# Optimization experiments

Measured on AMD Instinct MI355X. Metric: run time of the kernel, lower is better.

The kernel has to match this reference:

```python
import jax, jax.numpy as jnp
import numpy as np

N = 512          # pedestrians in scene
T = 12           # decode steps
OBS = 8
FEAT = 2
LAT = 32
COND = 64
LSTM_IN = 128
HID = 64         # lstm_hidden_size == context_state_size
CTX = 64
EMB = 32         # Pooling_net spatial embedding dim
MLP_IN = EMB + 2 * CTX   # 160
MLP_MID = 64
BOT = CTX        # bottleneck_dim = h_dim
IN_DEC = COND + LAT + CTX + FEAT  # 162


def setup_inputs() -> dict:
    key = jax.random.key(0)
    ks = jax.random.split(key, 24)
    s = 0.1
    return {
        "last_position": jax.random.normal(ks[0], (N, FEAT), jnp.float32),
        "c": jax.random.normal(ks[1], (N, COND), jnp.float32),
        "z": jax.random.normal(ks[2], (N, LAT), jnp.float32),
        "obs_traj_pos": jax.random.normal(ks[3], (OBS, N, FEAT), jnp.float32),
        "nei_index": jax.random.randint(ks[4], (T, N, N), 0, 2, jnp.int32),
        "nei_num_index": jax.random.randint(ks[5], (N,), 0, N, jnp.int32),
        "h0": jax.random.normal(ks[6], (N, HID), jnp.float32),
        "c0": jax.random.normal(ks[7], (N, HID), jnp.float32),
        "eps": jax.random.normal(ks[8], (T, N, FEAT), jnp.float32),
        "W_in": jax.random.normal(ks[9], (IN_DEC, LSTM_IN), jnp.float32) * s,
        "b_in": jnp.zeros((LSTM_IN,), jnp.float32),
        "W_ih": jax.random.normal(ks[10], (4 * HID, LSTM_IN), jnp.float32) * s,
        "W_hh": jax.random.normal(ks[11], (4 * HID, HID), jnp.float32) * s,
        "b_ih": jnp.zeros((4 * HID,), jnp.float32),
        "b_hh": jnp.zeros((4 * HID,), jnp.float32),
        "W_l2p": jax.random.normal(ks[12], (HID // 2 + CTX, FEAT), jnp.float32) * s,
        "b_l2p": jnp.zeros((FEAT,), jnp.float32),
        "W_sp": jax.random.normal(ks[13], (FEAT, EMB), jnp.float32) * s,
        "b_sp": jnp.zeros((EMB,), jnp.float32),
        "W1": jax.random.normal(ks[14], (MLP_IN, MLP_MID), jnp.float32) * s,
        "b1": jnp.zeros((MLP_MID,), jnp.float32),
        "W2": jax.random.normal(ks[15], (MLP_MID, BOT), jnp.float32) * s,
        "b2": jnp.zeros((BOT,), jnp.float32),
    }


def reference(last_position, c, z, obs_traj_pos, nei_index, nei_num_index,
              h0, c0, eps, W_in, b_in, W_ih, W_hh, b_ih, b_hh,
              W_l2p, b_l2p, W_sp, b_sp, W1, b1, W2, b2):
    sg = jax.lax.stop_gradient
    half = HID // 2
    neg_inf = jnp.float32(-jnp.inf)

    def pooling(mask, lstm_state, pos):
        # mask: [N,N] bool; lstm_state: [N,CTX]; pos: [N,2]
        corr = pos[:, None, :] - pos[None, :, :]           # [N,N,2] pos[i]-pos[j]
        r = corr @ W_sp + b_sp                              # [N,N,EMB]
        hj = jnp.broadcast_to(lstm_state[None, :, :], (N, N, CTX))
        hi = jnp.broadcast_to(lstm_state[:, None, :], (N, N, CTX))
        x = jnp.concatenate([r, hj, hi], axis=-1)           # [N,N,160]
        h1 = jax.nn.relu(x @ W1 + b1)
        h2 = jax.nn.relu(h1 @ W2 + b2)                      # [N,N,BOT]
        Hm = jnp.where(mask[:, :, None], h2, neg_inf)       # scatter of valid rows
        pool = Hm.max(axis=1)                               # max over neighbors j
        return jnp.where(pool == neg_inf, 0.0, pool)

    def lstm_cell(x, h, cs):
        gates = x @ W_ih.T + b_ih + h @ W_hh.T + b_hh
        i, f, g, o = jnp.split(gates, 4, axis=-1)
        c_new = jax.nn.sigmoid(f) * cs + jax.nn.sigmoid(i) * jnp.tanh(g)
        h_new = jax.nn.sigmoid(o) * jnp.tanh(c_new)
        return h_new, c_new

    def step(carry, xs):
        prev_pos, h, cs, ctx, cur_abs = carry
        nei_t, eps_t = xs
        emb = jnp.concatenate([sg(prev_pos), sg(c), sg(z), sg(ctx)], axis=-1)
        x = jax.nn.relu(emb @ W_in + b_in)
        h, cs = lstm_cell(x, h, cs)
        ctx = pooling(nei_t > 0, h, cur_abs)
        mu = jnp.concatenate([h[:, :half], ctx], -1) @ W_l2p + b_l2p
        logvar = jnp.concatenate([h[:, half:], ctx], -1) @ W_l2p + b_l2p
        pos = mu + eps_t * jnp.exp(0.5 * logvar)
        cur_abs = sg(cur_abs + pos)
        return (pos, h, cs, ctx, cur_abs), (pos, mu, logvar)

    ctx0 = jnp.zeros((N, CTX), jnp.float32)
    carry0 = (last_position, h0, c0, ctx0, obs_traj_pos[-1])
    _, (pre_pos, mean, var) = jax.lax.scan(step, carry0, (nei_index, eps))
    return pre_pos, mean, var
```

## Files before the change

kernel.cpp:

```cpp
#include <hip/hip_runtime.h>
#include <math.h>

#define NP 512
#define TT 12

typedef float f32x4 __attribute__((ext_vector_type(4)));
typedef __bf16 bf16x8 __attribute__((ext_vector_type(8)));

#define OFF_CURABS 0
#define OFF_Q      2048
#define OFF_P      67584
#define OFF_WIHT   100352
#define OFF_WHHT   133120
#define OFF_WC     149504
#define OFF_BASE   149632
#define OFF_H      149696
#define OFF_CS     182464

__global__ __launch_bounds__(256) void init_k(
    const float* __restrict__ obs, const float* __restrict__ W_ih,
    const float* __restrict__ W_hh, const float* __restrict__ W_sp,
    const float* __restrict__ b_sp, const float* __restrict__ W1,
    const float* __restrict__ b1, float* __restrict__ ws) {
  int tid = blockIdx.x * 256 + threadIdx.x;
  if (tid < 1024) ws[OFF_CURABS + tid] = obs[7 * 1024 + tid];
  if (tid < 32768) {
    int k = tid >> 8, g = tid & 255;
    ws[OFF_WIHT + tid] = W_ih[g * 128 + k];
  }
  if (tid < 16384) {
    int k = tid >> 8, g = tid & 255;
    ws[OFF_WHHT + tid] = W_hh[g * 64 + k];
  }
  if (tid < 128) {
    int d = tid >> 6, m = tid & 63;
    float s = 0.f;
    for (int e = 0; e < 32; ++e) s = fmaf(W_sp[d * 32 + e], W1[e * 64 + m], s);
    ws[OFF_WC + tid] = s;
  }
  if (tid < 64) {
    float s = b1[tid];
    for (int e = 0; e < 32; ++e) s = fmaf(b_sp[e], W1[e * 64 + tid], s);
    ws[OFF_BASE + tid] = s;
  }
}

__global__ __launch_bounds__(256) void step_k(
    const float* __restrict__ lastpos, const float* __restrict__ cc,
    const float* __restrict__ zz, const int* __restrict__ nei,
    const float* __restrict__ h0, const float* __restrict__ c0,
    const float* __restrict__ obs, const float* __restrict__ epsin,
    const float* __restrict__ W_in, const float* __restrict__ b_in,
    const float* __restrict__ b_ih, const float* __restrict__ b_hh,
    const float* __restrict__ Wl2p, const float* __restrict__ bl2p,
    const float* __restrict__ W1, const float* __restrict__ W2,
    const float* __restrict__ b2,
    float* __restrict__ out, float* __restrict__ ws, int s) {
  __shared__ __align__(16) __bf16 W2T[64 * 72];
  __shared__ int   ml[512];
  __shared__ float wcl[128], basev[64];
  __shared__ float red[4][64];
  __shared__ float hloc[64], csloc[64], ctxloc[64], prevp[2], pxy[2];
  __shared__ float emb[162], xpart[2][128], xvec[128], gl[256];

  int t = threadIdx.x;
  int b = blockIdx.x;
  int lane = t & 63, w = t >> 6;
  int quad = lane >> 4, col = lane & 15;

  if (t < 64) {
    if (s == 0) { hloc[t] = h0[b * 64 + t]; csloc[t] = c0[b * 64 + t]; ctxloc[t] = 0.f; }
    else        { hloc[t] = ws[OFF_H + b * 64 + t]; csloc[t] = ws[OFF_CS + b * 64 + t]; }
    basev[t] = ws[OFF_BASE + t];
  } else if (t < 192) {
    wcl[t - 64] = ws[OFF_WC + (t - 64)];
  }
  if (s == 0 && t < 2) {
    prevp[t] = lastpos[b * 2 + t];
    pxy[t]   = obs[7 * 1024 + b * 2 + t];
  }
  if (s > 0) {
    for (int e = t; e < 4096; e += 256)
      W2T[(e & 63) * 72 + (e >> 6)] = (__bf16)W2[e];
    const int* neirow = nei + ((size_t)(s - 1) * NP + b) * NP;
    for (int j = t; j < 512; j += 256) ml[j] = neirow[j];
  }
  __syncthreads();

  if (s > 0) {
    int st = s - 1;
    const float* Qb = ws + OFF_Q + (st & 1) * 32768;
    bf16x8 bf00 = *(const bf16x8*)&W2T[(0 * 16 + col) * 72 + 0 * 32 + quad * 8];
    bf16x8 bf01 = *(const bf16x8*)&W2T[(0 * 16 + col) * 72 + 1 * 32 + quad * 8];
    bf16x8 bf10 = *(const bf16x8*)&W2T[(1 * 16 + col) * 72 + 0 * 32 + quad * 8];
    bf16x8 bf11 = *(const bf16x8*)&W2T[(1 * 16 + col) * 72 + 1 * 32 + quad * 8];
    bf16x8 bf20 = *(const bf16x8*)&W2T[(2 * 16 + col) * 72 + 0 * 32 + quad * 8];
    bf16x8 bf21 = *(const bf16x8*)&W2T[(2 * 16 + col) * 72 + 1 * 32 + quad * 8];
    bf16x8 bf30 = *(const bf16x8*)&W2T[(3 * 16 + col) * 72 + 0 * 32 + quad * 8];
    bf16x8 bf31 = *(const bf16x8*)&W2T[(3 * 16 + col) * 72 + 1 * 32 + quad * 8];
    float pl0[8], pl1[8];
    #pragma unroll
    for (int e = 0; e < 8; ++e) {
      pl0[e] = ws[OFF_P + b * 64 + quad * 8 + e];
      pl1[e] = ws[OFF_P + b * 64 + 32 + quad * 8 + e];
    }
    float vmax0 = -1e30f, vmax1 = -1e30f, vmax2 = -1e30f, vmax3 = -1e30f;

    for (int c = 0; c < 8; ++c) {
      int j0 = w * 128 + c * 16;
      int jr = (j0 + col) * 64 + quad * 8;
      f32x4 qa = *(const f32x4*)&Qb[jr];
      f32x4 qb = *(const f32x4*)&Qb[jr + 4];
      f32x4 qc = *(const f32x4*)&Qb[jr + 32];
      f32x4 qd = *(const f32x4*)&Qb[jr + 36];
      bf16x8 a0, a1;
      #pragma unroll
      for (int e = 0; e < 4; ++e) {
        a0[e]     = (__bf16)fmaxf(qa[e] + pl0[e],     0.f);
        a0[e + 4] = (__bf16)fmaxf(qb[e] + pl0[e + 4], 0.f);
        a1[e]     = (__bf16)fmaxf(qc[e] + pl1[e],     0.f);
        a1[e + 4] = (__bf16)fmaxf(qd[e] + pl1[e + 4], 0.f);
      }
      int mrow = j0 + quad * 4;
      bool mk0 = ml[mrow] > 0, mk1 = ml[mrow + 1] > 0,
           mk2 = ml[mrow + 2] > 0, mk3 = ml[mrow + 3] > 0;
      f32x4 acc;
      acc = (f32x4){0.f, 0.f, 0.f, 0.f};
      acc = __builtin_amdgcn_mfma_f32_16x16x32_bf16(a0, bf00, acc, 0, 0, 0);
      acc = __builtin_amdgcn_mfma_f32_16x16x32_bf16(a1, bf01, acc, 0, 0, 0);
      vmax0 = fmaxf(vmax0, mk0 ? acc[0] : -1e30f);
      vmax0 = fmaxf(vmax0, mk1 ? acc[1] : -1e30f);
      vmax0 = fmaxf(vmax0, mk2 ? acc[2] : -1e30f);
      vmax0 = fmaxf(vmax0, mk3 ? acc[3] : -1e30f);
      acc = (f32x4){0.f, 0.f, 0.f, 0.f};
      acc = __builtin_amdgcn_mfma_f32_16x16x32_bf16(a0, bf10, acc, 0, 0, 0);
      acc = __builtin_amdgcn_mfma_f32_16x16x32_bf16(a1, bf11, acc, 0, 0, 0);
      vmax1 = fmaxf(vmax1, mk0 ? acc[0] : -1e30f);
      vmax1 = fmaxf(vmax1, mk1 ? acc[1] : -1e30f);
      vmax1 = fmaxf(vmax1, mk2 ? acc[2] : -1e30f);
      vmax1 = fmaxf(vmax1, mk3 ? acc[3] : -1e30f);
      acc = (f32x4){0.f, 0.f, 0.f, 0.f};
      acc = __builtin_amdgcn_mfma_f32_16x16x32_bf16(a0, bf20, acc, 0, 0, 0);
      acc = __builtin_amdgcn_mfma_f32_16x16x32_bf16(a1, bf21, acc, 0, 0, 0);
      vmax2 = fmaxf(vmax2, mk0 ? acc[0] : -1e30f);
      vmax2 = fmaxf(vmax2, mk1 ? acc[1] : -1e30f);
      vmax2 = fmaxf(vmax2, mk2 ? acc[2] : -1e30f);
      vmax2 = fmaxf(vmax2, mk3 ? acc[3] : -1e30f);
      acc = (f32x4){0.f, 0.f, 0.f, 0.f};
      acc = __builtin_amdgcn_mfma_f32_16x16x32_bf16(a0, bf30, acc, 0, 0, 0);
      acc = __builtin_amdgcn_mfma_f32_16x16x32_bf16(a1, bf31, acc, 0, 0, 0);
      vmax3 = fmaxf(vmax3, mk0 ? acc[0] : -1e30f);
      vmax3 = fmaxf(vmax3, mk1 ? acc[1] : -1e30f);
      vmax3 = fmaxf(vmax3, mk2 ? acc[2] : -1e30f);
      vmax3 = fmaxf(vmax3, mk3 ? acc[3] : -1e30f);
    }
    vmax0 = fmaxf(vmax0, __shfl_xor(vmax0, 16));
    vmax0 = fmaxf(vmax0, __shfl_xor(vmax0, 32));
    vmax1 = fmaxf(vmax1, __shfl_xor(vmax1, 16));
    vmax1 = fmaxf(vmax1, __shfl_xor(vmax1, 32));
    vmax2 = fmaxf(vmax2, __shfl_xor(vmax2, 16));
    vmax2 = fmaxf(vmax2, __shfl_xor(vmax2, 32));
    vmax3 = fmaxf(vmax3, __shfl_xor(vmax3, 16));
    vmax3 = fmaxf(vmax3, __shfl_xor(vmax3, 32));
    if (lane < 16) {
      red[w][0 * 16 + lane] = vmax0;
      red[w][1 * 16 + lane] = vmax1;
      red[w][2 * 16 + lane] = vmax2;
      red[w][3 * 16 + lane] = vmax3;
    }
    __syncthreads();
    if (t < 64) {
      float m4 = fmaxf(fmaxf(red[0][t], red[1][t]),
                       fmaxf(red[2][t], red[3][t]));
      ctxloc[t] = fmaxf(m4 + b2[t], 0.f);
    }
    __syncthreads();
    if (t < 64) {
      int l = t;
      float cl = ctxloc[l];
      float sc0 = cl * Wl2p[(32 + l) * 2 + 0];
      float sc1 = cl * Wl2p[(32 + l) * 2 + 1];
      float m0 = 0.f, m1 = 0.f, v0 = 0.f, v1 = 0.f;
      if (l < 32) {
        float hm = hloc[l];
        m0 = hm * Wl2p[l * 2 + 0]; m1 = hm * Wl2p[l * 2 + 1];
        float hv = hloc[32 + l];
        v0 = hv * Wl2p[l * 2 + 0]; v1 = hv * Wl2p[l * 2 + 1];
      }
      for (int off = 32; off >= 1; off >>= 1) {
        sc0 += __shfl_down(sc0, off);
        sc1 += __shfl_down(sc1, off);
        m0  += __shfl_down(m0,  off);
        m1  += __shfl_down(m1,  off);
        v0  += __shfl_down(v0,  off);
        v1  += __shfl_down(v1,  off);
      }
      if (l == 0) {
        float mu0 = m0 + sc0 + bl2p[0], mu1 = m1 + sc1 + bl2p[1];
        float lv0 = v0 + sc0 + bl2p[0], lv1 = v1 + sc1 + bl2p[1];
        float e0 = epsin[st * 1024 + b * 2 + 0];
        float e1 = epsin[st * 1024 + b * 2 + 1];
        float p0 = mu0 + e0 * expf(0.5f * lv0);
        float p1 = mu1 + e1 * expf(0.5f * lv1);
        out[st * 1024 + b * 2 + 0] = p0;
        out[st * 1024 + b * 2 + 1] = p1;
        out[12288 + st * 1024 + b * 2 + 0] = mu0;
        out[12288 + st * 1024 + b * 2 + 1] = mu1;
        out[24576 + st * 1024 + b * 2 + 0] = lv0;
        out[24576 + st * 1024 + b * 2 + 1] = lv1;
        float px = ws[OFF_CURABS + (st & 1) * 1024 + b * 2 + 0];
        float py = ws[OFF_CURABS + (st & 1) * 1024 + b * 2 + 1];
        float nx = px + p0, ny = py + p1;
        ws[OFF_CURABS + ((st & 1) ^ 1) * 1024 + b * 2 + 0] = nx;
        ws[OFF_CURABS + ((st & 1) ^ 1) * 1024 + b * 2 + 1] = ny;
        pxy[0] = nx; pxy[1] = ny;
        prevp[0] = p0; prevp[1] = p1;
      }
    }
    __syncthreads();
  }

  if (s < TT) {
    if (t < 162) {
      float v;
      if (t < 2)       v = prevp[t];
      else if (t < 66) v = cc[b * 64 + (t - 2)];
      else if (t < 98) v = zz[b * 32 + (t - 66)];
      else             v = ctxloc[t - 98];
      emb[t] = v;
    }
    __syncthreads();
    {
      int k = t & 127, p = t >> 7;
      float a0 = 0.f, a1 = 0.f;
      int d = p;
      for (; d + 2 < 162; d += 4) {
        a0 = fmaf(emb[d],     W_in[d * 128 + k],       a0);
        a1 = fmaf(emb[d + 2], W_in[(d + 2) * 128 + k], a1);
      }
      if (d < 162) a0 = fmaf(emb[d], W_in[d * 128 + k], a0);
      xpart[p][k] = a0 + a1;
    }
    __syncthreads();
    if (t < 128) xvec[t] = fmaxf(xpart[0][t] + xpart[1][t] + b_in[t], 0.f);
    __syncthreads();
    {
      int g = t;
      const float* wiht = ws + OFF_WIHT;
      const float* whht = ws + OFF_WHHT;
      float s0 = 0.f, s1 = 0.f, s2 = 0.f, s3 = 0.f;
      for (int kk = 0; kk < 128; kk += 4) {
        s0 = fmaf(xvec[kk],     wiht[kk * 256 + g],       s0);
        s1 = fmaf(xvec[kk + 1], wiht[(kk + 1) * 256 + g], s1);
        s2 = fmaf(xvec[kk + 2], wiht[(kk + 2) * 256 + g], s2);
        s3 = fmaf(xvec[kk + 3], wiht[(kk + 3) * 256 + g], s3);
      }
      for (int kk = 0; kk < 64; kk += 4) {
        s0 = fmaf(hloc[kk],     whht[kk * 256 + g],       s0);
        s1 = fmaf(hloc[kk + 1], whht[(kk + 1) * 256 + g], s1);
        s2 = fmaf(hloc[kk + 2], whht[(kk + 2) * 256 + g], s2);
        s3 = fmaf(hloc[kk + 3], whht[(kk + 3) * 256 + g], s3);
      }
      gl[g] = b_ih[g] + b_hh[g] + ((s0 + s1) + (s2 + s3));
    }
    __syncthreads();
    if (t < 64) {
      float ig = gl[t], fg = gl[64 + t], gg = gl[128 + t], og = gl[192 + t];
      float is = 1.f / (1.f + expf(-ig));
      float fs = 1.f / (1.f + expf(-fg));
      float os = 1.f / (1.f + expf(-og));
      float cn = fs * csloc[t] + is * tanhf(gg);
      float hv = os * tanhf(cn);
      hloc[t] = hv;
      ws[OFF_CS + b * 64 + t] = cn;
      ws[OFF_H + b * 64 + t] = hv;
    }
    __syncthreads();
    if (t < 128) {
      int which = t >> 6, m = t & 63;
      const float* wb = W1 + (32 + which * 64) * 64 + m;
      float s0 = 0.f, s1 = 0.f, s2 = 0.f, s3 = 0.f;
      for (int k = 0; k < 64; k += 4) {
        s0 = fmaf(hloc[k],     wb[k * 64],       s0);
        s1 = fmaf(hloc[k + 1], wb[(k + 1) * 64], s1);
        s2 = fmaf(hloc[k + 2], wb[(k + 2) * 64], s2);
        s3 = fmaf(hloc[k + 3], wb[(k + 3) * 64], s3);
      }
      float sv = (s0 + s1) + (s2 + s3);
      float cx = pxy[0], cy = pxy[1];
      if (which == 0)
        ws[OFF_Q + (s & 1) * 32768 + b * 64 + m] =
            sv + basev[m] - cx * wcl[m] - cy * wcl[64 + m];
      else
        ws[OFF_P + b * 64 + m] = sv + cx * wcl[m] + cy * wcl[64 + m];
    }
  }
}

extern "C" void kernel_launch(void* const* d_in, const int* in_sizes, int n_in,
                              void* d_out, int out_size, void* d_ws, size_t ws_size,
                              hipStream_t stream) {
  const float* lastpos = (const float*)d_in[0];
  const float* cc      = (const float*)d_in[1];
  const float* zz      = (const float*)d_in[2];
  const float* obs     = (const float*)d_in[3];
  const int*   nei     = (const int*)d_in[4];
  const float* h0      = (const float*)d_in[6];
  const float* c0      = (const float*)d_in[7];
  const float* eps     = (const float*)d_in[8];
  const float* W_in    = (const float*)d_in[9];
  const float* b_in    = (const float*)d_in[10];
  const float* W_ih    = (const float*)d_in[11];
  const float* W_hh    = (const float*)d_in[12];
  const float* b_ih    = (const float*)d_in[13];
  const float* b_hh    = (const float*)d_in[14];
  const float* W_l2p   = (const float*)d_in[15];
  const float* b_l2p   = (const float*)d_in[16];
  const float* W_sp    = (const float*)d_in[17];
  const float* b_sp    = (const float*)d_in[18];
  const float* W1      = (const float*)d_in[19];
  const float* b1      = (const float*)d_in[20];
  const float* W2      = (const float*)d_in[21];
  const float* b2      = (const float*)d_in[22];
  float* out = (float*)d_out;
  float* ws  = (float*)d_ws;

  hipLaunchKernelGGL(init_k, dim3(128), dim3(256), 0, stream,
                     obs, W_ih, W_hh, W_sp, b_sp, W1, b1, ws);
  for (int s = 0; s <= TT; ++s) {
    hipLaunchKernelGGL(step_k, dim3(NP), dim3(256), 0, stream,
                       lastpos, cc, zz, nei, h0, c0, obs, eps,
                       W_in, b_in, b_ih, b_hh, W_l2p, b_l2p,
                       W1, W2, b2, out, ws, s);
  }
}
```

Baseline: 369.4 us.

## Precompute step-invariant c/z input projection and store recurrent weights as bf16

The c and z parts of the input embedding do not change across steps, so their product with W_in is computed once per pedestrian in init_k and read back each step. Only the position and context terms are recomputed. The LSTM gate weights, the context slice of W_in and the W1 slices are stored as bf16 in workspace to halve the bytes each of the 512 blocks reads per step. This trades weight precision for less global memory traffic and adds 512 blocks of setup work to init_k.

```diff
diff --git a/kernel.cpp b/kernel.cpp
--- a/kernel.cpp
+++ b/kernel.cpp
@@ -10,58 +10,79 @@
 #define OFF_CURABS 0
 #define OFF_Q      2048
 #define OFF_P      67584
-#define OFF_WIHT   100352
-#define OFF_WHHT   133120
-#define OFF_WC     149504
-#define OFF_BASE   149632
-#define OFF_H      149696
-#define OFF_CS     182464
+#define OFF_H      100352
+#define OFF_CS     133120
+#define OFF_XCZ    165888
+#define OFF_WGB    231424
+#define OFF_WCTXB  256000
+#define OFF_W1B    260096
+#define OFF_WIN01  264192
+#define OFF_WC     264448
+#define OFF_BASE   264576
 
 __global__ __launch_bounds__(256) void init_k(
-    const float* __restrict__ obs, const float* __restrict__ W_ih,
+    const float* __restrict__ obs, const float* __restrict__ cc,
+    const float* __restrict__ zz,
+    const float* __restrict__ W_in, const float* __restrict__ W_ih,
     const float* __restrict__ W_hh, const float* __restrict__ W_sp,
     const float* __restrict__ b_sp, const float* __restrict__ W1,
     const float* __restrict__ b1, float* __restrict__ ws) {
-  int tid = blockIdx.x * 256 + threadIdx.x;
-  if (tid < 1024) ws[OFF_CURABS + tid] = obs[7 * 1024 + tid];
-  if (tid < 32768) {
-    int k = tid >> 8, g = tid & 255;
-    ws[OFF_WIHT + tid] = W_ih[g * 128 + k];
-  }
-  if (tid < 16384) {
-    int k = tid >> 8, g = tid & 255;
-    ws[OFF_WHHT + tid] = W_hh[g * 64 + k];
-  }
-  if (tid < 128) {
-    int d = tid >> 6, m = tid & 63;
-    float s = 0.f;
-    for (int e = 0; e < 32; ++e) s = fmaf(W_sp[d * 32 + e], W1[e * 64 + m], s);
-    ws[OFF_WC + tid] = s;
-  }
-  if (tid < 64) {
-    float s = b1[tid];
-    for (int e = 0; e < 32; ++e) s = fmaf(b_sp[e], W1[e * 64 + tid], s);
-    ws[OFF_BASE + tid] = s;
+  if (blockIdx.x < 128) {
+    int id = blockIdx.x * 256 + threadIdx.x;
+    if (id < 1024) ws[OFF_CURABS + id] = obs[7 * 1024 + id];
+    __bf16* wgb = (__bf16*)(ws + OFF_WGB);
+    for (int e = id; e < 49152; e += 32768) {
+      int k = e >> 8, g = e & 255;
+      float v = (k < 128) ? W_ih[g * 128 + k] : W_hh[g * 64 + (k - 128)];
+      wgb[e] = (__bf16)v;
+    }
+    if (id < 8192) {
+      int d = id >> 7, k = id & 127;
+      ((__bf16*)(ws + OFF_WCTXB))[id] = (__bf16)W_in[(98 + d) * 128 + k];
+    }
+    if (id < 8192) {
+      int r = id >> 6, m = id & 63;
+      ((__bf16*)(ws + OFF_W1B))[id] = (__bf16)W1[(32 + r) * 64 + m];
+    }
+    if (id < 256) ws[OFF_WIN01 + id] = W_in[(id >> 7) * 128 + (id & 127)];
+    if (id < 128) {
+      int d = id >> 6, m = id & 63;
+      float s = 0.f;
+      for (int e = 0; e < 32; ++e) s = fmaf(W_sp[d * 32 + e], W1[e * 64 + m], s);
+      ws[OFF_WC + id] = s;
+    }
+    if (id < 64) {
+      float s = b1[id];
+      for (int e = 0; e < 32; ++e) s = fmaf(b_sp[e], W1[e * 64 + id], s);
+      ws[OFF_BASE + id] = s;
+    }
+  } else {
+    int b = blockIdx.x - 128;
+    int k = threadIdx.x;
+    if (k < 128) {
+      float s = 0.f;
+      for (int d = 0; d < 64; ++d) s = fmaf(cc[b * 64 + d], W_in[(2 + d) * 128 + k], s);
+      for (int d = 0; d < 32; ++d) s = fmaf(zz[b * 32 + d], W_in[(66 + d) * 128 + k], s);
+      ws[OFF_XCZ + b * 128 + k] = s;
+    }
   }
 }
 
 __global__ __launch_bounds__(256) void step_k(
-    const float* __restrict__ lastpos, const float* __restrict__ cc,
-    const float* __restrict__ zz, const int* __restrict__ nei,
+    const float* __restrict__ lastpos, const int* __restrict__ nei,
     const float* __restrict__ h0, const float* __restrict__ c0,
     const float* __restrict__ obs, const float* __restrict__ epsin,
-    const float* __restrict__ W_in, const float* __restrict__ b_in,
+    const float* __restrict__ b_in,
     const float* __restrict__ b_ih, const float* __restrict__ b_hh,
     const float* __restrict__ Wl2p, const float* __restrict__ bl2p,
-    const float* __restrict__ W1, const float* __restrict__ W2,
-    const float* __restrict__ b2,
+    const float* __restrict__ W2, const float* __restrict__ b2,
     float* __restrict__ out, float* __restrict__ ws, int s) {
   __shared__ __align__(16) __bf16 W2T[64 * 72];
   __shared__ int   ml[512];
   __shared__ float wcl[128], basev[64];
   __shared__ float red[4][64];
   __shared__ float hloc[64], csloc[64], ctxloc[64], prevp[2], pxy[2];
-  __shared__ float emb[162], xpart[2][128], xvec[128], gl[256];
+  __shared__ float xpart[2][128], xvec[128], gl[256];
 
   int t = threadIdx.x;
   int b = blockIdx.x;
@@ -221,24 +242,19 @@
   }
 
   if (s < TT) {
-    if (t < 162) {
-      float v;
-      if (t < 2)       v = prevp[t];
-      else if (t < 66) v = cc[b * 64 + (t - 2)];
-      else if (t < 98) v = zz[b * 32 + (t - 66)];
-      else             v = ctxloc[t - 98];
-      emb[t] = v;
-    }
-    __syncthreads();
     {
       int k = t & 127, p = t >> 7;
+      const __bf16* wctx = (const __bf16*)(ws + OFF_WCTXB);
       float a0 = 0.f, a1 = 0.f;
+      if (p == 0)
+        a0 = ws[OFF_XCZ + b * 128 + k] +
+             prevp[0] * ws[OFF_WIN01 + k] + prevp[1] * ws[OFF_WIN01 + 128 + k];
       int d = p;
-      for (; d + 2 < 162; d += 4) {
-        a0 = fmaf(emb[d],     W_in[d * 128 + k],       a0);
-        a1 = fmaf(emb[d + 2], W_in[(d + 2) * 128 + k], a1);
-      }
-      if (d < 162) a0 = fmaf(emb[d], W_in[d * 128 + k], a0);
+      for (; d + 2 < 64; d += 4) {
+        a0 = fmaf(ctxloc[d],     (float)wctx[d * 128 + k],       a0);
+        a1 = fmaf(ctxloc[d + 2], (float)wctx[(d + 2) * 128 + k], a1);
+      }
+      if (d < 64) a0 = fmaf(ctxloc[d], (float)wctx[d * 128 + k], a0);
       xpart[p][k] = a0 + a1;
     }
     __syncthreads();
@@ -246,20 +262,19 @@
     __syncthreads();
     {
       int g = t;
-      const float* wiht = ws + OFF_WIHT;
-      const float* whht = ws + OFF_WHHT;
+      const __bf16* wgb = (const __bf16*)(ws + OFF_WGB);
       float s0 = 0.f, s1 = 0.f, s2 = 0.f, s3 = 0.f;
       for (int kk = 0; kk < 128; kk += 4) {
-        s0 = fmaf(xvec[kk],     wiht[kk * 256 + g],       s0);
-        s1 = fmaf(xvec[kk + 1], wiht[(kk + 1) * 256 + g], s1);
-        s2 = fmaf(xvec[kk + 2], wiht[(kk + 2) * 256 + g], s2);
-        s3 = fmaf(xvec[kk + 3], wiht[(kk + 3) * 256 + g], s3);
+        s0 = fmaf(xvec[kk],     (float)wgb[kk * 256 + g],       s0);
+        s1 = fmaf(xvec[kk + 1], (float)wgb[(kk + 1) * 256 + g], s1);
+        s2 = fmaf(xvec[kk + 2], (float)wgb[(kk + 2) * 256 + g], s2);
+        s3 = fmaf(xvec[kk + 3], (float)wgb[(kk + 3) * 256 + g], s3);
       }
       for (int kk = 0; kk < 64; kk += 4) {
-        s0 = fmaf(hloc[kk],     whht[kk * 256 + g],       s0);
-        s1 = fmaf(hloc[kk + 1], whht[(kk + 1) * 256 + g], s1);
-        s2 = fmaf(hloc[kk + 2], whht[(kk + 2) * 256 + g], s2);
-        s3 = fmaf(hloc[kk + 3], whht[(kk + 3) * 256 + g], s3);
+        s0 = fmaf(hloc[kk],     (float)wgb[(128 + kk) * 256 + g],     s0);
+        s1 = fmaf(hloc[kk + 1], (float)wgb[(129 + kk) * 256 + g],     s1);
+        s2 = fmaf(hloc[kk + 2], (float)wgb[(130 + kk) * 256 + g],     s2);
+        s3 = fmaf(hloc[kk + 3], (float)wgb[(131 + kk) * 256 + g],     s3);
       }
       gl[g] = b_ih[g] + b_hh[g] + ((s0 + s1) + (s2 + s3));
     }
@@ -278,13 +293,13 @@
     __syncthreads();
     if (t < 128) {
       int which = t >> 6, m = t & 63;
-      const float* wb = W1 + (32 + which * 64) * 64 + m;
+      const __bf16* wb = (const __bf16*)(ws + OFF_W1B) + which * 4096 + m;
       float s0 = 0.f, s1 = 0.f, s2 = 0.f, s3 = 0.f;
       for (int k = 0; k < 64; k += 4) {
-        s0 = fmaf(hloc[k],     wb[k * 64],       s0);
-        s1 = fmaf(hloc[k + 1], wb[(k + 1) * 64], s1);
-        s2 = fmaf(hloc[k + 2], wb[(k + 2) * 64], s2);
-        s3 = fmaf(hloc[k + 3], wb[(k + 3) * 64], s3);
+        s0 = fmaf(hloc[k],     (float)wb[k * 64],       s0);
+        s1 = fmaf(hloc[k + 1], (float)wb[(k + 1) * 64], s1);
+        s2 = fmaf(hloc[k + 2], (float)wb[(k + 2) * 64], s2);
+        s3 = fmaf(hloc[k + 3], (float)wb[(k + 3) * 64], s3);
       }
       float sv = (s0 + s1) + (s2 + s3);
       float cx = pxy[0], cy = pxy[1];
@@ -325,12 +340,12 @@
   float* out = (float*)d_out;
   float* ws  = (float*)d_ws;
 
-  hipLaunchKernelGGL(init_k, dim3(128), dim3(256), 0, stream,
-                     obs, W_ih, W_hh, W_sp, b_sp, W1, b1, ws);
+  hipLaunchKernelGGL(init_k, dim3(640), dim3(256), 0, stream,
+                     obs, cc, zz, W_in, W_ih, W_hh, W_sp, b_sp, W1, b1, ws);
   for (int s = 0; s <= TT; ++s) {
     hipLaunchKernelGGL(step_k, dim3(NP), dim3(256), 0, stream,
-                       lastpos, cc, zz, nei, h0, c0, obs, eps,
-                       W_in, b_in, b_ih, b_hh, W_l2p, b_l2p,
-                       W1, W2, b2, out, ws, s);
+                       lastpos, nei, h0, c0, obs, eps,
+                       b_in, b_ih, b_hh, W_l2p, b_l2p,
+                       W2, b2, out, ws, s);
   }
 }
```

New measurement: 335.3 us. 9.2% less time.
